# Performance work log

Hardware: AMD Instinct MI355X
Metric: run time of the kernel (lower is better)

Reference implementation:

```python
import jax, jax.numpy as jnp
import numpy as np

C_Z, H, C = 128, 4, 32
L = 320
SCALE = 1.0 / np.sqrt(C)
EPS = 1e-5


def setup_inputs() -> dict:
    key = jax.random.key(0)
    ks = jax.random.split(key, 8)
    s = 0.02
    return {
        "z": jax.random.normal(ks[0], (L, L, C_Z), dtype=jnp.float32),
        "pair_mask": jnp.ones((L, L), dtype=jnp.float32),
        "res_mask": jnp.ones((L,), dtype=bool),
        "ln_gamma": jnp.ones((C_Z,), dtype=jnp.float32),
        "ln_beta": jnp.zeros((C_Z,), dtype=jnp.float32),
        "Wq": jax.random.normal(ks[1], (C_Z, H * C), dtype=jnp.float32) * s,
        "Wk": jax.random.normal(ks[2], (C_Z, H * C), dtype=jnp.float32) * s,
        "Wv": jax.random.normal(ks[3], (C_Z, H * C), dtype=jnp.float32) * s,
        "Wb": jax.random.normal(ks[4], (C_Z, H), dtype=jnp.float32) * s,
        "Wg": jax.random.normal(ks[5], (C_Z, H * C), dtype=jnp.float32) * s,
        "Wout": jax.random.normal(ks[6], (H * C, C_Z), dtype=jnp.float32) * s,
    }


def _layernorm(x, gamma, beta):
    mu = jnp.mean(x, axis=-1, keepdims=True)
    var = jnp.mean(jnp.square(x - mu), axis=-1, keepdims=True)
    return (x - mu) * jax.lax.rsqrt(var + EPS) * gamma + beta


def reference(z, pair_mask, res_mask, ln_gamma, ln_beta, Wq, Wk, Wv, Wb, Wg, Wout):
    Ldim = z.shape[0]
    z_ln = _layernorm(z, ln_gamma, ln_beta)                      # [L,L,c_z]
    Q = (z_ln @ Wq).reshape(Ldim, Ldim, H, C)                    # [i,j,h,c]
    K = (z_ln @ Wk).reshape(Ldim, Ldim, H, C)                    # [i,k,h,c]
    V = (z_ln @ Wv).reshape(Ldim, Ldim, H, C)                    # [i,k,h,c]
    B = z_ln @ Wb                                                # [j,k,h]
    G = jax.nn.sigmoid(z_ln @ Wg).reshape(Ldim, Ldim, H, C)      # [i,j,h,c]

    # logits[i,h,j,k] = <Q[i,j], K[i,k]> * scale + B[j,k,h]
    logits = jnp.einsum("ijhc,ikhc->ihjk", Q, K) * SCALE
    logits = logits + jnp.transpose(B, (2, 0, 1))[None]          # +[1,h,j,k]
    neg_inf = jnp.asarray(-jnp.inf, logits.dtype)
    logits = jnp.where(res_mask[None, None, None, :], logits, neg_inf)
    attn = jax.nn.softmax(logits, axis=-1)                       # over k

    out = jnp.einsum("ihjk,ikhc->ijhc", attn, V)                 # [i,j,h,c]
    out = (G * out).reshape(Ldim, Ldim, H * C)
    dz = out @ Wout                                              # [L,L,c_z]
    return dz * pair_mask[..., None]
```

## Files before the change

### kernel.cpp

```cpp
#include <hip/hip_runtime.h>

#define LDIM 320
#define CZ 128
#define NH 4
#define CH 32
#define SCALE2F (0.17677669529663687f * 1.4426950408889634f)
#define LOG2E 1.4426950408889634f
#define LN_EPS 1e-5f

typedef __attribute__((ext_vector_type(8))) short bf16x8;
typedef __attribute__((ext_vector_type(4))) float f32x4;

__device__ __forceinline__ unsigned int pack_bf2(float a, float b) {
  unsigned int ua = __float_as_uint(a);
  unsigned int ub = __float_as_uint(b);
  unsigned int ra = (ua + 0x7fffu + ((ua >> 16) & 1u)) >> 16;
  unsigned int rb = (ub + 0x7fffu + ((ub >> 16) & 1u)) >> 16;
  return (ra & 0xffffu) | (rb << 16);
}

__device__ __forceinline__ unsigned short f2bf(float a) {
  unsigned int ua = __float_as_uint(a);
  return (unsigned short)((ua + 0x7fffu + ((ua >> 16) & 1u)) >> 16);
}

__device__ __forceinline__ float bf2f(unsigned short u) {
  return __uint_as_float(((unsigned int)u) << 16);
}

__device__ __forceinline__ unsigned cvtpk(float a, float b) {
  unsigned r;
  asm("v_cvt_pk_bf16_f32 %0, %1, %2" : "=v"(r) : "v"(a), "v"(b));
  return r;
}

__global__ __launch_bounds__(256) void k_prep(
    const float* __restrict__ Wq, const float* __restrict__ Wk,
    const float* __restrict__ Wv, const float* __restrict__ Wb,
    const float* __restrict__ Wg, const float* __restrict__ Wout,
    unsigned short* __restrict__ Wt, unsigned short* __restrict__ Woutt)
{
  __shared__ __attribute__((aligned(16))) unsigned short buf[64 * 136];
  const int t = threadIdx.x, bid = blockIdx.x;
  const bool isOut = (bid >= 9);
  const int n0 = isOut ? (bid - 9) * 64 : bid * 64;
  const int nl = t & 63;
  const int n = n0 + nl;
#pragma unroll 8
  for (int it = 0; it < 32; ++it) {
    const int k = (t >> 6) + 4 * it;
    float v;
    if (isOut)        v = Wout[k * 128 + n];
    else if (n < 128) v = Wq[k * 128 + n];
    else if (n < 256) v = Wk[k * 128 + n - 128];
    else if (n < 384) v = Wv[k * 128 + n - 256];
    else if (n < 512) v = Wg[k * 128 + n - 384];
    else if (n < 516) v = Wb[k * 4 + n - 512];
    else              v = 0.f;
    buf[nl * 136 + k] = f2bf(v);
  }
  __syncthreads();
  unsigned short* dst = isOut ? Woutt : Wt;
#pragma unroll
  for (int it = 0; it < 4; ++it) {
    const int idx = t + 256 * it;
    const int rr = idx >> 4, ck = idx & 15;
    const uint4 d = *(const uint4*)&buf[rr * 136 + ck * 8];
    *(uint4*)(dst + (size_t)(n0 + rr) * 128 + ck * 8) = d;
  }
}

__global__ __launch_bounds__(256) void k_lnproj(
    const float* __restrict__ z, const float* __restrict__ gamma,
    const float* __restrict__ beta, const unsigned short* __restrict__ Wt,
    const int* __restrict__ rmask,
    unsigned short* __restrict__ Qg, unsigned short* __restrict__ Kg,
    unsigned short* __restrict__ Vg, unsigned short* __restrict__ Gg,
    float* __restrict__ Bh)
{
  __shared__ __attribute__((aligned(16))) unsigned short As[128 * 136];
  const int t = threadIdx.x;
  const int m0 = blockIdx.x * 128;
  const int rlane = t & 7;

  const float* gp = gamma + rlane * 16;
  const float* bp = beta + rlane * 16;
  const float4 g0 = *(const float4*)(gp + 0);
  const float4 g1 = *(const float4*)(gp + 4);
  const float4 g2 = *(const float4*)(gp + 8);
  const float4 g3 = *(const float4*)(gp + 12);
  const float4 b0 = *(const float4*)(bp + 0);
  const float4 b1 = *(const float4*)(bp + 4);
  const float4 b2 = *(const float4*)(bp + 8);
  const float4 b3 = *(const float4*)(bp + 12);

#pragma unroll
  for (int rr = 0; rr < 4; ++rr) {
    const int row = rr * 32 + (t >> 3);
    const float* zp = z + (size_t)(m0 + row) * CZ + rlane * 16;
    const float4 x0 = *(const float4*)(zp + 0);
    const float4 x1 = *(const float4*)(zp + 4);
    const float4 x2 = *(const float4*)(zp + 8);
    const float4 x3 = *(const float4*)(zp + 12);
    float s  = x0.x + x0.y + x0.z + x0.w + x1.x + x1.y + x1.z + x1.w +
               x2.x + x2.y + x2.z + x2.w + x3.x + x3.y + x3.z + x3.w;
    float ss = x0.x*x0.x + x0.y*x0.y + x0.z*x0.z + x0.w*x0.w +
               x1.x*x1.x + x1.y*x1.y + x1.z*x1.z + x1.w*x1.w +
               x2.x*x2.x + x2.y*x2.y + x2.z*x2.z + x2.w*x2.w +
               x3.x*x3.x + x3.y*x3.y + x3.z*x3.z + x3.w*x3.w;
    s  += __shfl_xor(s, 1);  ss += __shfl_xor(ss, 1);
    s  += __shfl_xor(s, 2);  ss += __shfl_xor(ss, 2);
    s  += __shfl_xor(s, 4);  ss += __shfl_xor(ss, 4);
    const float mu  = s * (1.f / 128.f);
    const float var = ss * (1.f / 128.f) - mu * mu;
    const float rs  = rsqrtf(var + LN_EPS);
    uint4 u0, u1;
    u0.x = pack_bf2((x0.x - mu) * rs * g0.x + b0.x, (x0.y - mu) * rs * g0.y + b0.y);
    u0.y = pack_bf2((x0.z - mu) * rs * g0.z + b0.z, (x0.w - mu) * rs * g0.w + b0.w);
    u0.z = pack_bf2((x1.x - mu) * rs * g1.x + b1.x, (x1.y - mu) * rs * g1.y + b1.y);
    u0.w = pack_bf2((x1.z - mu) * rs * g1.z + b1.z, (x1.w - mu) * rs * g1.w + b1.w);
    u1.x = pack_bf2((x2.x - mu) * rs * g2.x + b2.x, (x2.y - mu) * rs * g2.y + b2.y);
    u1.y = pack_bf2((x2.z - mu) * rs * g2.z + b2.z, (x2.w - mu) * rs * g2.w + b2.w);
    u1.z = pack_bf2((x3.x - mu) * rs * g3.x + b3.x, (x3.y - mu) * rs * g3.y + b3.y);
    u1.w = pack_bf2((x3.z - mu) * rs * g3.z + b3.z, (x3.w - mu) * rs * g3.w + b3.w);
    unsigned short* dst = &As[row * 136 + rlane * 16];
    *(uint4*)(dst + 0) = u0;
    *(uint4*)(dst + 8) = u1;
  }
  __syncthreads();

  const int w = t >> 6, lane = t & 63;
  const int m16 = lane & 15, qd = lane >> 4;
  const f32x4 z4 = {0.f, 0.f, 0.f, 0.f};

  bf16x8 af[2][4];
#pragma unroll
  for (int ks = 0; ks < 4; ++ks) {
    af[0][ks] = *(const bf16x8*)&As[(w * 32 + m16) * 136 + ks * 32 + qd * 8];
    af[1][ks] = *(const bf16x8*)&As[(w * 32 + 16 + m16) * 136 + ks * 32 + qd * 8];
  }

  for (int ntile = 0; ntile < 8; ++ntile) {
    f32x4 acc[2][4];
#pragma unroll
    for (int sub = 0; sub < 2; ++sub)
#pragma unroll
      for (int nt = 0; nt < 4; ++nt) acc[sub][nt] = z4;
#pragma unroll
    for (int ks = 0; ks < 4; ++ks) {
#pragma unroll
      for (int nt = 0; nt < 4; ++nt) {
        const bf16x8 bf = *(const bf16x8*)(
            Wt + (size_t)(ntile * 64 + m16 * 4 + nt) * 128 + ks * 32 + qd * 8);
        acc[0][nt] = __builtin_amdgcn_mfma_f32_16x16x32_bf16(af[0][ks], bf, acc[0][nt], 0, 0, 0);
        acc[1][nt] = __builtin_amdgcn_mfma_f32_16x16x32_bf16(af[1][ks], bf, acc[1][nt], 0, 0, 0);
      }
    }
    const int cc0 = (m16 * 4) & 31;
    const int hh = (ntile & 1) * 2 + (m16 >> 3);
    unsigned short* dstb =
        (ntile < 2 ? Qg : (ntile < 4 ? Kg : (ntile < 6 ? Vg : Gg)));
#pragma unroll
    for (int sub = 0; sub < 2; ++sub) {
#pragma unroll
      for (int r = 0; r < 4; ++r) {
        const int p = m0 + w * 32 + sub * 16 + qd * 4 + r;
        const int a = p / 320, bb = p - a * 320;
        float v0 = acc[sub][0][r], v1 = acc[sub][1][r];
        float v2 = acc[sub][2][r], v3 = acc[sub][3][r];
        if (ntile >= 6) {
          v0 = 1.f / (1.f + __expf(-v0));
          v1 = 1.f / (1.f + __expf(-v1));
          v2 = 1.f / (1.f + __expf(-v2));
          v3 = 1.f / (1.f + __expf(-v3));
        }
        uint2 pk;
        pk.x = pack_bf2(v0, v1);
        pk.y = pack_bf2(v2, v3);
        *(uint2*)(dstb + ((size_t)(a * 4 + hh) * 320 + bb) * 32 + cc0) = pk;
      }
    }
  }

  {
    f32x4 acc0 = z4, acc1 = z4;
#pragma unroll
    for (int ks = 0; ks < 4; ++ks) {
      const bf16x8 bf = *(const bf16x8*)(
          Wt + (size_t)(512 + m16) * 128 + ks * 32 + qd * 8);
      acc0 = __builtin_amdgcn_mfma_f32_16x16x32_bf16(af[0][ks], bf, acc0, 0, 0, 0);
      acc1 = __builtin_amdgcn_mfma_f32_16x16x32_bf16(af[1][ks], bf, acc1, 0, 0, 0);
    }
    if (m16 < 4) {
#pragma unroll
      for (int r = 0; r < 4; ++r) {
        const int p0 = m0 + w * 32 + qd * 4 + r;
        const int p1 = p0 + 16;
        const float mk0 = rmask[p0 % 320] ? 0.f : -INFINITY;
        const float mk1 = rmask[p1 % 320] ? 0.f : -INFINITY;
        Bh[(size_t)m16 * 102400 + p0] = acc0[r] * LOG2E + mk0;
        Bh[(size_t)m16 * 102400 + p1] = acc1[r] * LOG2E + mk1;
      }
    }
  }
}

__global__ __launch_bounds__(256) void k_attn(
    const unsigned short* __restrict__ Qg, const unsigned short* __restrict__ Kg,
    const unsigned short* __restrict__ Vg, const unsigned short* __restrict__ Gg,
    const float* __restrict__ Bh, unsigned short* __restrict__ Obg)
{
  __shared__ __attribute__((aligned(16))) unsigned short Vt[32 * 328];
  __shared__ __attribute__((aligned(16))) unsigned short Ps[4][16 * 168];
  const int h = blockIdx.x, i = blockIdx.y;
  const int t = threadIdx.x;
  const size_t base = (size_t)(i * NH + h) * (LDIM * CH);

  {
    const int k0 = t >> 3, c4 = (t & 7) * 4;
#pragma unroll
    for (int it = 0; it < 10; ++it) {
      const int k = k0 + 32 * it;
      const uint2 d = *(const uint2*)(Vg + base + k * 32 + c4);
      Vt[(c4 + 0) * 328 + k] = (unsigned short)(d.x & 0xffffu);
      Vt[(c4 + 1) * 328 + k] = (unsigned short)(d.x >> 16);
      Vt[(c4 + 2) * 328 + k] = (unsigned short)(d.y & 0xffffu);
      Vt[(c4 + 3) * 328 + k] = (unsigned short)(d.y >> 16);
    }
  }
  __syncthreads();

  const int w = t >> 6, lane = t & 63;
  const int m16 = lane & 15, qd = lane >> 4;
  const f32x4 z4 = {0.f, 0.f, 0.f, 0.f};

  for (int jt = w; jt < 20; jt += 4) {
    const bf16x8 qfrag =
        *(const bf16x8*)(Qg + base + (size_t)(jt * 16 + m16) * 32 + qd * 8);

    f32x4 acc[20];
    __builtin_amdgcn_s_setprio(1);
#pragma unroll
    for (int kt = 0; kt < 20; ++kt) {
      const bf16x8 kf =
          *(const bf16x8*)(Kg + base + (size_t)(kt * 16 + m16) * 32 + qd * 8);
      acc[kt] = __builtin_amdgcn_mfma_f32_16x16x32_bf16(kf, qfrag, z4, 0, 0, 0);
    }
    __builtin_amdgcn_s_setprio(0);

    const float* bq = Bh + (size_t)h * 102400 +
                      (size_t)(jt * 16 + m16) * 320 + qd * 4;
    float mx[4] = {-INFINITY, -INFINITY, -INFINITY, -INFINITY};
#pragma unroll
    for (int kt = 0; kt < 20; ++kt) {
      const float4 bv = *(const float4*)(bq + kt * 16);
      const float s0 = fmaf(acc[kt][0], SCALE2F, bv.x);
      const float s1 = fmaf(acc[kt][1], SCALE2F, bv.y);
      const float s2 = fmaf(acc[kt][2], SCALE2F, bv.z);
      const float s3 = fmaf(acc[kt][3], SCALE2F, bv.w);
      acc[kt][0] = s0; acc[kt][1] = s1; acc[kt][2] = s2; acc[kt][3] = s3;
      mx[0] = fmaxf(mx[0], s0);
      mx[1] = fmaxf(mx[1], s1);
      mx[2] = fmaxf(mx[2], s2);
      mx[3] = fmaxf(mx[3], s3);
    }
    float mxx = fmaxf(fmaxf(mx[0], mx[1]), fmaxf(mx[2], mx[3]));
    mxx = fmaxf(mxx, __shfl_xor(mxx, 16));
    mxx = fmaxf(mxx, __shfl_xor(mxx, 32));

    float l0 = 0.f, l1 = 0.f, l2 = 0.f, l3 = 0.f;
#pragma unroll
    for (int kt = 0; kt < 20; ++kt) {
      const float p0 = __builtin_amdgcn_exp2f(acc[kt][0] - mxx);
      const float p1 = __builtin_amdgcn_exp2f(acc[kt][1] - mxx);
      const float p2 = __builtin_amdgcn_exp2f(acc[kt][2] - mxx);
      const float p3 = __builtin_amdgcn_exp2f(acc[kt][3] - mxx);
      acc[kt][0] = p0; acc[kt][1] = p1; acc[kt][2] = p2; acc[kt][3] = p3;
      l0 += p0; l1 += p1; l2 += p2; l3 += p3;
    }
    float l = (l0 + l1) + (l2 + l3);
    l += __shfl_xor(l, 16);
    l += __shfl_xor(l, 32);
    const float rl = __builtin_amdgcn_rcpf(l);

    f32x4 accO0 = z4, accO1 = z4;
#pragma unroll
    for (int hh = 0; hh < 2; ++hh) {
#pragma unroll
      for (int kt2 = 0; kt2 < 10; ++kt2) {
        const int kt = hh * 10 + kt2;
        uint2 wv;
        wv.x = cvtpk(acc[kt][0], acc[kt][1]);
        wv.y = cvtpk(acc[kt][2], acc[kt][3]);
        *(uint2*)&Ps[w][m16 * 168 + kt2 * 16 + qd * 4] = wv;
      }
      __builtin_amdgcn_s_setprio(1);
#pragma unroll
      for (int ks = 0; ks < 5; ++ks) {
        const bf16x8 pf = *(const bf16x8*)&Ps[w][m16 * 168 + ks * 32 + qd * 8];
        const bf16x8 v0 =
            *(const bf16x8*)&Vt[m16 * 328 + hh * 160 + ks * 32 + qd * 8];
        const bf16x8 v1 =
            *(const bf16x8*)&Vt[(16 + m16) * 328 + hh * 160 + ks * 32 + qd * 8];
        accO0 = __builtin_amdgcn_mfma_f32_16x16x32_bf16(v0, pf, accO0, 0, 0, 0);
        accO1 = __builtin_amdgcn_mfma_f32_16x16x32_bf16(v1, pf, accO1, 0, 0, 0);
      }
      __builtin_amdgcn_s_setprio(0);
    }

    {
      const int j = jt * 16 + m16;
      const uint2 gg0 = *(const uint2*)(Gg + base + (size_t)j * 32 + qd * 4);
      const uint2 gg1 = *(const uint2*)(Gg + base + (size_t)j * 32 + 16 + qd * 4);
      const float ga0 = bf2f((unsigned short)(gg0.x & 0xffffu));
      const float ga1 = bf2f((unsigned short)(gg0.x >> 16));
      const float ga2 = bf2f((unsigned short)(gg0.y & 0xffffu));
      const float ga3 = bf2f((unsigned short)(gg0.y >> 16));
      const float gb0 = bf2f((unsigned short)(gg1.x & 0xffffu));
      const float gb1 = bf2f((unsigned short)(gg1.x >> 16));
      const float gb2 = bf2f((unsigned short)(gg1.y & 0xffffu));
      const float gb3 = bf2f((unsigned short)(gg1.y >> 16));
      unsigned short* op = Obg + (size_t)(i * 320 + j) * 128 + h * 32;
      uint2 o0, o1;
      o0.x = cvtpk(ga0 * rl * accO0[0], ga1 * rl * accO0[1]);
      o0.y = cvtpk(ga2 * rl * accO0[2], ga3 * rl * accO0[3]);
      o1.x = cvtpk(gb0 * rl * accO1[0], gb1 * rl * accO1[1]);
      o1.y = cvtpk(gb2 * rl * accO1[2], gb3 * rl * accO1[3]);
      *(uint2*)(op + qd * 4) = o0;
      *(uint2*)(op + 16 + qd * 4) = o1;
    }
  }
}

__global__ __launch_bounds__(256) void k_out(
    const unsigned short* __restrict__ Obg, const unsigned short* __restrict__ Woutt,
    const float* __restrict__ pm, float* __restrict__ out)
{
  __shared__ __attribute__((aligned(16))) unsigned short As[128 * 136];
  __shared__ __attribute__((aligned(16))) unsigned short Bs[64 * 136];
  const int t = threadIdx.x;
  const int ntile = blockIdx.x;
  const int m0 = blockIdx.y * 128;

#pragma unroll
  for (int it = 0; it < 8; ++it) {
    const int idx = t + 256 * it;
    const int rr = idx >> 4, ck = idx & 15;
    const uint4 d = *(const uint4*)(Obg + (size_t)(m0 + rr) * 128 + ck * 8);
    *(uint4*)&As[rr * 136 + ck * 8] = d;
  }
  {
    const unsigned short* wrow = Woutt + (size_t)ntile * 64 * 128;
#pragma unroll
    for (int it = 0; it < 4; ++it) {
      const int idx = t + 256 * it;
      const int n = idx >> 4, ck = idx & 15;
      const uint4 d = *(const uint4*)(wrow + n * 128 + ck * 8);
      *(uint4*)&Bs[n * 136 + ck * 8] = d;
    }
  }
  __syncthreads();

  const int w = t >> 6, lane = t & 63;
  const int m16 = lane & 15, qd = lane >> 4;
  const f32x4 z4 = {0.f, 0.f, 0.f, 0.f};
  f32x4 acc[2][4];
#pragma unroll
  for (int sub = 0; sub < 2; ++sub)
#pragma unroll
    for (int nt = 0; nt < 4; ++nt) acc[sub][nt] = z4;

#pragma unroll
  for (int ks = 0; ks < 4; ++ks) {
    const bf16x8 af0 = *(const bf16x8*)&As[(w * 32 + m16) * 136 + qd * 8 + ks * 32];
    const bf16x8 af1 = *(const bf16x8*)&As[(w * 32 + 16 + m16) * 136 + qd * 8 + ks * 32];
#pragma unroll
    for (int nt = 0; nt < 4; ++nt) {
      const bf16x8 bf = *(const bf16x8*)&Bs[(nt * 16 + m16) * 136 + qd * 8 + ks * 32];
      acc[0][nt] = __builtin_amdgcn_mfma_f32_16x16x32_bf16(af0, bf, acc[0][nt], 0, 0, 0);
      acc[1][nt] = __builtin_amdgcn_mfma_f32_16x16x32_bf16(af1, bf, acc[1][nt], 0, 0, 0);
    }
  }

#pragma unroll
  for (int sub = 0; sub < 2; ++sub) {
#pragma unroll
    for (int r = 0; r < 4; ++r) {
      const int p = m0 + w * 32 + sub * 16 + qd * 4 + r;
      const float m = pm[p];
      float* orow = out + (size_t)p * 128 + ntile * 64;
#pragma unroll
      for (int nt = 0; nt < 4; ++nt)
        orow[nt * 16 + m16] = acc[sub][nt][r] * m;
    }
  }
}

extern "C" void kernel_launch(void* const* d_in, const int* in_sizes, int n_in,
                              void* d_out, int out_size, void* d_ws, size_t ws_size,
                              hipStream_t stream)
{
  const float* z     = (const float*)d_in[0];
  const float* pmask = (const float*)d_in[1];
  const int*   rmask = (const int*)d_in[2];
  const float* gamma = (const float*)d_in[3];
  const float* beta  = (const float*)d_in[4];
  const float* Wq    = (const float*)d_in[5];
  const float* Wk    = (const float*)d_in[6];
  const float* Wv    = (const float*)d_in[7];
  const float* Wb    = (const float*)d_in[8];
  const float* Wg    = (const float*)d_in[9];
  const float* Wout  = (const float*)d_in[10];

  const size_t P = (size_t)LDIM * LDIM;
  const size_t E = P * 128;
  char* ws = (char*)d_ws;
  unsigned short* Qg = (unsigned short*)ws;
  unsigned short* Kg = Qg + E;
  unsigned short* Vg = Kg + E;
  unsigned short* Gg = Vg + E;
  unsigned short* Obg = Gg + E;
  unsigned short* Wt = Obg + E;
  unsigned short* Woutt = Wt + 576 * 128;
  float* Bh = (float*)(Woutt + 128 * 128);

  k_prep<<<dim3(11), 256, 0, stream>>>(Wq, Wk, Wv, Wb, Wg, Wout, Wt, Woutt);
  k_lnproj<<<dim3(800), 256, 0, stream>>>(z, gamma, beta, Wt, rmask,
                                          Qg, Kg, Vg, Gg, Bh);
  k_attn<<<dim3(NH, LDIM), 256, 0, stream>>>(Qg, Kg, Vg, Gg, Bh, Obg);
  k_out<<<dim3(2, 800), 256, 0, stream>>>(Obg, Woutt, pmask, (float*)d_out);
}
```

Measured before the change: 340.7 us.

## Swizzle attention LDS layouts, add occupancy hint, drop LDS staging in output GEMM

```diff
diff --git a/kernel.cpp b/kernel.cpp
--- a/kernel.cpp
+++ b/kernel.cpp
@@ -205,16 +205,18 @@
   }
 }
 
-__global__ __launch_bounds__(256) void k_attn(
+__global__ __launch_bounds__(256, 4) void k_attn(
     const unsigned short* __restrict__ Qg, const unsigned short* __restrict__ Kg,
     const unsigned short* __restrict__ Vg, const unsigned short* __restrict__ Gg,
     const float* __restrict__ Bh, unsigned short* __restrict__ Obg)
 {
-  __shared__ __attribute__((aligned(16))) unsigned short Vt[32 * 328];
-  __shared__ __attribute__((aligned(16))) unsigned short Ps[4][16 * 168];
+  __shared__ __attribute__((aligned(16))) unsigned short Vt[32 * 320];
+  __shared__ __attribute__((aligned(16))) unsigned short Psz[16 * 4 * 160];
   const int h = blockIdx.x, i = blockIdx.y;
   const int t = threadIdx.x;
   const size_t base = (size_t)(i * NH + h) * (LDIM * CH);
+  char* const vtb = (char*)Vt;
+  char* const psb = (char*)Psz;
 
   {
     const int k0 = t >> 3, c4 = (t & 7) * 4;
@@ -222,16 +224,21 @@
     for (int it = 0; it < 10; ++it) {
       const int k = k0 + 32 * it;
       const uint2 d = *(const uint2*)(Vg + base + k * 32 + c4);
-      Vt[(c4 + 0) * 328 + k] = (unsigned short)(d.x & 0xffffu);
-      Vt[(c4 + 1) * 328 + k] = (unsigned short)(d.x >> 16);
-      Vt[(c4 + 2) * 328 + k] = (unsigned short)(d.y & 0xffffu);
-      Vt[(c4 + 3) * 328 + k] = (unsigned short)(d.y >> 16);
+      *(unsigned short*)(vtb + ((((c4 + 0) * 640) + k * 2) ^ (((c4 + 0) & 7) << 4))) =
+          (unsigned short)(d.x & 0xffffu);
+      *(unsigned short*)(vtb + ((((c4 + 1) * 640) + k * 2) ^ (((c4 + 1) & 7) << 4))) =
+          (unsigned short)(d.x >> 16);
+      *(unsigned short*)(vtb + ((((c4 + 2) * 640) + k * 2) ^ (((c4 + 2) & 7) << 4))) =
+          (unsigned short)(d.y & 0xffffu);
+      *(unsigned short*)(vtb + ((((c4 + 3) * 640) + k * 2) ^ (((c4 + 3) & 7) << 4))) =
+          (unsigned short)(d.y >> 16);
     }
   }
   __syncthreads();
 
   const int w = t >> 6, lane = t & 63;
   const int m16 = lane & 15, qd = lane >> 4;
+  const int swv = (m16 & 7) << 4;
   const f32x4 z4 = {0.f, 0.f, 0.f, 0.f};
 
   for (int jt = w; jt < 20; jt += 4) {
@@ -292,16 +299,17 @@
         uint2 wv;
         wv.x = cvtpk(acc[kt][0], acc[kt][1]);
         wv.y = cvtpk(acc[kt][2], acc[kt][3]);
-        *(uint2*)&Ps[w][m16 * 168 + kt2 * 16 + qd * 4] = wv;
+        *(uint2*)(psb + ((m16 * 1280 + w * 320 + kt2 * 32 + qd * 8) ^ swv)) = wv;
       }
       __builtin_amdgcn_s_setprio(1);
 #pragma unroll
       for (int ks = 0; ks < 5; ++ks) {
-        const bf16x8 pf = *(const bf16x8*)&Ps[w][m16 * 168 + ks * 32 + qd * 8];
-        const bf16x8 v0 =
-            *(const bf16x8*)&Vt[m16 * 328 + hh * 160 + ks * 32 + qd * 8];
-        const bf16x8 v1 =
-            *(const bf16x8*)&Vt[(16 + m16) * 328 + hh * 160 + ks * 32 + qd * 8];
+        const bf16x8 pf = *(const bf16x8*)(
+            psb + ((m16 * 1280 + w * 320 + ks * 64 + qd * 16) ^ swv));
+        const bf16x8 v0 = *(const bf16x8*)(
+            vtb + ((m16 * 640 + (hh * 160 + ks * 32 + qd * 8) * 2) ^ swv));
+        const bf16x8 v1 = *(const bf16x8*)(
+            vtb + (((16 + m16) * 640 + (hh * 160 + ks * 32 + qd * 8) * 2) ^ swv));
         accO0 = __builtin_amdgcn_mfma_f32_16x16x32_bf16(v0, pf, accO0, 0, 0, 0);
         accO1 = __builtin_amdgcn_mfma_f32_16x16x32_bf16(v1, pf, accO1, 0, 0, 0);
       }
@@ -336,31 +344,9 @@
     const unsigned short* __restrict__ Obg, const unsigned short* __restrict__ Woutt,
     const float* __restrict__ pm, float* __restrict__ out)
 {
-  __shared__ __attribute__((aligned(16))) unsigned short As[128 * 136];
-  __shared__ __attribute__((aligned(16))) unsigned short Bs[64 * 136];
   const int t = threadIdx.x;
   const int ntile = blockIdx.x;
   const int m0 = blockIdx.y * 128;
-
-#pragma unroll
-  for (int it = 0; it < 8; ++it) {
-    const int idx = t + 256 * it;
-    const int rr = idx >> 4, ck = idx & 15;
-    const uint4 d = *(const uint4*)(Obg + (size_t)(m0 + rr) * 128 + ck * 8);
-    *(uint4*)&As[rr * 136 + ck * 8] = d;
-  }
-  {
-    const unsigned short* wrow = Woutt + (size_t)ntile * 64 * 128;
-#pragma unroll
-    for (int it = 0; it < 4; ++it) {
-      const int idx = t + 256 * it;
-      const int n = idx >> 4, ck = idx & 15;
-      const uint4 d = *(const uint4*)(wrow + n * 128 + ck * 8);
-      *(uint4*)&Bs[n * 136 + ck * 8] = d;
-    }
-  }
-  __syncthreads();
-
   const int w = t >> 6, lane = t & 63;
   const int m16 = lane & 15, qd = lane >> 4;
   const f32x4 z4 = {0.f, 0.f, 0.f, 0.f};
@@ -372,11 +358,14 @@
 
 #pragma unroll
   for (int ks = 0; ks < 4; ++ks) {
-    const bf16x8 af0 = *(const bf16x8*)&As[(w * 32 + m16) * 136 + qd * 8 + ks * 32];
-    const bf16x8 af1 = *(const bf16x8*)&As[(w * 32 + 16 + m16) * 136 + qd * 8 + ks * 32];
+    const bf16x8 af0 = *(const bf16x8*)(
+        Obg + (size_t)(m0 + w * 32 + m16) * 128 + ks * 32 + qd * 8);
+    const bf16x8 af1 = *(const bf16x8*)(
+        Obg + (size_t)(m0 + w * 32 + 16 + m16) * 128 + ks * 32 + qd * 8);
 #pragma unroll
     for (int nt = 0; nt < 4; ++nt) {
-      const bf16x8 bf = *(const bf16x8*)&Bs[(nt * 16 + m16) * 136 + qd * 8 + ks * 32];
+      const bf16x8 bf = *(const bf16x8*)(
+          Woutt + (size_t)(ntile * 64 + nt * 16 + m16) * 128 + ks * 32 + qd * 8);
       acc[0][nt] = __builtin_amdgcn_mfma_f32_16x16x32_bf16(af0, bf, acc[0][nt], 0, 0, 0);
       acc[1][nt] = __builtin_amdgcn_mfma_f32_16x16x32_bf16(af1, bf, acc[1][nt], 0, 0, 0);
     }
```

New measurement: 512.1 us. 1.5x slower.
